# Kernel optimization log

Hardware: AMD Instinct MI355X
Metric: run time of the kernel (lower is better)

The kernel has to match this reference:

```python
import jax, jax.numpy as jnp
import numpy as np

B, S, D, E, R, TOP_K = 4, 4096, 1024, 10, 4, 2
SCALING = 1.0 / R  # alpha / rank


def setup_inputs() -> dict:
    key = jax.random.key(0)
    ks = jax.random.split(key, 7)
    return {
        "x": jax.random.normal(ks[0], (B, S, D), dtype=jnp.float32),
        "W_base": jax.random.normal(ks[1], (D, D), dtype=jnp.float32) * (D ** -0.5),
        "b_base": jax.random.normal(ks[2], (D,), dtype=jnp.float32) * 0.02,
        "gate_W": jax.random.normal(ks[3], (E, D), dtype=jnp.float32) * (D ** -0.5),
        "gate_b": jax.random.normal(ks[4], (E,), dtype=jnp.float32) * 0.02,
        "lora_down": jax.random.normal(ks[5], (E, R, D), dtype=jnp.float32) * (D ** -0.5),
        "lora_up": jax.random.normal(ks[6], (E, D, R), dtype=jnp.float32) * (R ** -0.5),
    }


def reference(x, W_base, b_base, gate_W, gate_b, lora_down, lora_up):
    # Base (frozen) linear: [B,S,D]
    base_out = jnp.einsum("bsd,od->bso", x, W_base) + b_base

    # Top-k gating: logits [B,S,E] -> sparse softmax weights [B,S,E]
    logits = jnp.einsum("bsd,ed->bse", x, gate_W) + gate_b
    top_vals, top_idx = jax.lax.top_k(logits, TOP_K)          # [B,S,K]
    top_w = jax.nn.softmax(top_vals, axis=-1)                 # [B,S,K]
    # scatter top-k weights back to dense [B,S,E] (non-top-k are zero)
    weights = jnp.sum(top_w[..., None] * jax.nn.one_hot(top_idx, E, dtype=x.dtype), axis=-2)

    # All-expert LoRA (matches original loop); weight in rank space to avoid
    # materializing [B,S,E,D]: sum_e w_e * up_e(down_e(x)) * scaling
    h = jnp.einsum("bsd,erd->bser", x, lora_down)             # [B,S,E,R]
    h = h * weights[..., None]
    lora_out = jnp.einsum("bser,edr->bsd", h, lora_up) * SCALING

    return base_out + lora_out
```

## Files before the change

kernel.cpp:

```cpp
#include <hip/hip_runtime.h>
#include <hip/hip_bf16.h>
#include <cstdint>
#include <cstddef>

#define D_DIM 1024
#define E_NUM 10

typedef __attribute__((ext_vector_type(8))) short bf16x8;
typedef __attribute__((ext_vector_type(4))) float f32x4;
typedef unsigned short u16;
typedef unsigned int u32;

__device__ __forceinline__ u16 f2bf(float f) {
  union { float f; u32 u; } v; v.f = f;
  u32 r = v.u + 0x7fffu + ((v.u >> 16) & 1u);
  return (u16)(r >> 16);
}
__device__ __forceinline__ float bf2f(u16 u) {
  union { u32 u; float f; } v; v.u = ((u32)u) << 16; return v.f;
}
__device__ __forceinline__ float dot4(float4 a, float4 b) {
  return a.x * b.x + a.y * b.y + a.z * b.z + a.w * b.w;
}

__global__ void conv_w(const float* __restrict__ W, u16* __restrict__ Wb) {
  const int i = (blockIdx.x * 256 + threadIdx.x) * 8;
  float4 a = *(const float4*)(W + i);
  float4 b = *(const float4*)(W + i + 4);
  *(ushort4*)(Wb + i)     = make_ushort4(f2bf(a.x), f2bf(a.y), f2bf(a.z), f2bf(a.w));
  *(ushort4*)(Wb + i + 4) = make_ushort4(f2bf(b.x), f2bf(b.y), f2bf(b.z), f2bf(b.w));
}

__global__ void prep_ldb(const float* __restrict__ ld, u16* __restrict__ Bld) {
  const int r = blockIdx.x;
  for (int c = threadIdx.x; c < D_DIM; c += 256)
    Bld[r * D_DIM + c] = (r < 40) ? f2bf(ld[r * D_DIM + c]) : (u16)0;
}

__global__ void prep_ub(const float* __restrict__ lup, u16* __restrict__ Ub) {
  const int g = blockIdx.x * 256 + threadIdx.x;
  const int o = g >> 6, j = g & 63;
  Ub[g] = (j < 40) ? f2bf(lup[(size_t)(j >> 2) * (D_DIM * 4) + o * 4 + (j & 3)]) : (u16)0;
}

__global__ __launch_bounds__(256)
void moe_prep_h(const float* __restrict__ x, const u16* __restrict__ Bld,
                u16* __restrict__ hb, u16* __restrict__ xb) {
  __shared__ u16 sX[4][16 * 64];
  __shared__ u16 sB[4][48 * 64];
  __shared__ float sP[4][3][16][17];

  const int tid = threadIdx.x, lane = tid & 63, w = tid >> 6;
  const int r0 = blockIdx.x * 16;
  const int kbase = w * 256;

  f32x4 acc[3] = {};

  float4 av[4];
#pragma unroll
  for (int i = 0; i < 2; ++i) {
    const int c = lane * 2 + i, row = c >> 3, kc = c & 7;
    const float* g = x + (size_t)(r0 + row) * D_DIM + kbase + kc * 8;
    av[i * 2]     = *(const float4*)g;
    av[i * 2 + 1] = *(const float4*)(g + 4);
  }

#pragma unroll 1
  for (int kt = 0; kt < 4; ++kt) {
    const int k0 = kbase + kt * 64;
#pragma unroll
    for (int i = 0; i < 6; ++i) {
      const int c = i * 64 + lane, row = c >> 3, kc = (c & 7) ^ (row & 7);
      __builtin_amdgcn_global_load_lds(
          (const __attribute__((address_space(1))) u32*)(Bld + (size_t)row * D_DIM + k0 + kc * 8),
          (__attribute__((address_space(3))) u32*)&sB[w][c * 8], 16, 0, 0);
    }
#pragma unroll
    for (int i = 0; i < 2; ++i) {
      const int c = lane * 2 + i, row = c >> 3, kc = c & 7;
      const float4 a = av[i * 2], b = av[i * 2 + 1];
      const ushort4 ha = make_ushort4(f2bf(a.x), f2bf(a.y), f2bf(a.z), f2bf(a.w));
      const ushort4 hb4 = make_ushort4(f2bf(b.x), f2bf(b.y), f2bf(b.z), f2bf(b.w));
      const int off = (row * 128 + kc * 16) ^ ((row & 7) << 4);
      *(ushort4*)((char*)sX[w] + off)     = ha;
      *(ushort4*)((char*)sX[w] + off + 8) = hb4;
      if (xb) {
        u16* dst = xb + (size_t)(r0 + row) * D_DIM + k0 + kc * 8;
        *(ushort4*)dst       = ha;
        *(ushort4*)(dst + 4) = hb4;
      }
    }
    __syncthreads();
    if (kt < 3) {
#pragma unroll
      for (int i = 0; i < 2; ++i) {
        const int c = lane * 2 + i, row = c >> 3, kc = c & 7;
        const float* g = x + (size_t)(r0 + row) * D_DIM + (k0 + 64) + kc * 8;
        av[i * 2]     = *(const float4*)g;
        av[i * 2 + 1] = *(const float4*)(g + 4);
      }
    }
#pragma unroll
    for (int kk = 0; kk < 2; ++kk) {
      const int kb = kk * 64 + ((lane >> 4) * 16);
      const int rA = lane & 15;
      const bf16x8 a0 = *(const bf16x8*)((const char*)sX[w] + ((rA * 128 + kb) ^ ((rA & 7) << 4)));
#pragma unroll
      for (int cf = 0; cf < 3; ++cf) {
        const int rB = cf * 16 + (lane & 15);
        const bf16x8 q = *(const bf16x8*)((const char*)sB[w] + ((rB * 128 + kb) ^ ((rB & 7) << 4)));
        acc[cf] = __builtin_amdgcn_mfma_f32_16x16x32_bf16(a0, q, acc[cf], 0, 0, 0);
      }
    }
    __syncthreads();
  }

#pragma unroll
  for (int cf = 0; cf < 3; ++cf)
#pragma unroll
    for (int j = 0; j < 4; ++j)
      sP[w][cf][(lane >> 4) * 4 + j][lane & 15] = acc[cf][j];
  __syncthreads();

  const int row = tid >> 4, c16 = tid & 15;
#pragma unroll
  for (int cf = 0; cf < 3; ++cf) {
    const int col = cf * 16 + c16;
    if (col < 40) {
      const float s = sP[0][cf][row][c16] + sP[1][cf][row][c16] +
                      sP[2][cf][row][c16] + sP[3][cf][row][c16];
      hb[(size_t)(r0 + row) * 40 + col] = f2bf(s);
    }
  }
}

__global__ __launch_bounds__(256, 2)
void moe_gate(const float* __restrict__ x, const float* __restrict__ gW,
              const float* __restrict__ gb, const u16* __restrict__ hb,
              u16* __restrict__ cd) {
  const int tid = threadIdx.x, lane = tid & 63, w = tid >> 6;
  const int tb = blockIdx.x * 16 + w * 4;

  float4 xv[4][4];
#pragma unroll
  for (int tok = 0; tok < 4; ++tok)
#pragma unroll
    for (int j = 0; j < 4; ++j)
      xv[tok][j] = *(const float4*)(x + (size_t)(tb + tok) * D_DIM + j * 256 + lane * 4);

  float lg[4][E_NUM];
#pragma unroll
  for (int e = 0; e < E_NUM; ++e) {
    float a0 = 0.f, a1 = 0.f, a2 = 0.f, a3 = 0.f;
#pragma unroll
    for (int j = 0; j < 4; ++j) {
      const float4 wv = *(const float4*)(gW + e * D_DIM + j * 256 + lane * 4);
      a0 += dot4(xv[0][j], wv);
      a1 += dot4(xv[1][j], wv);
      a2 += dot4(xv[2][j], wv);
      a3 += dot4(xv[3][j], wv);
    }
#pragma unroll
    for (int o = 32; o; o >>= 1) {
      a0 += __shfl_xor(a0, o);
      a1 += __shfl_xor(a1, o);
      a2 += __shfl_xor(a2, o);
      a3 += __shfl_xor(a3, o);
    }
    const float be = gb[e];
    lg[0][e] = a0 + be;
    lg[1][e] = a1 + be;
    lg[2][e] = a2 + be;
    lg[3][e] = a3 + be;
  }

  if (lane < 4) {
    const int tok = lane, t = tb + tok;
    int e0 = 0; float v0 = lg[tok][0];
#pragma unroll
    for (int e = 1; e < E_NUM; ++e) if (lg[tok][e] > v0) { v0 = lg[tok][e]; e0 = e; }
    int e1 = -1; float v1 = -3.0e38f;
#pragma unroll
    for (int e = 0; e < E_NUM; ++e) if (e != e0 && lg[tok][e] > v1) { v1 = lg[tok][e]; e1 = e; }
    const float pp = expf(v1 - v0);
    const float inv = 1.f / (1.f + pp);
    const float s0 = inv * 0.25f, s1 = pp * inv * 0.25f;

    u16* dst = cd + (size_t)t * 64;
    const u16* hrow = hb + (size_t)t * 40;
#pragma unroll
    for (int e = 0; e < E_NUM; ++e) {
      const float we = (e == e0) ? s0 : ((e == e1) ? s1 : 0.f);
      const ushort4 hh = *(const ushort4*)(hrow + e * 4);
      *(ushort4*)(dst + e * 4) = make_ushort4(
          f2bf(bf2f(hh.x) * we), f2bf(bf2f(hh.y) * we),
          f2bf(bf2f(hh.z) * we), f2bf(bf2f(hh.w) * we));
    }
#pragma unroll
    for (int j = 40; j < 64; j += 4)
      *(ushort4*)(dst + j) = make_ushort4(0, 0, 0, 0);
  }
}

__global__ __launch_bounds__(256, 2)
void moe_gemm_t(const u16* __restrict__ xb, const u16* __restrict__ Wbf,
                const u16* __restrict__ cd, const u16* __restrict__ Ub,
                const float* __restrict__ bias, float* __restrict__ out) {
  __shared__ u16 Al[2][128 * 64];
  __shared__ u16 Bl[2][128 * 64];

  const int tid = threadIdx.x, lane = tid & 63, wid = tid >> 6;
  const int wm = wid >> 1, wn = wid & 1;
  const int p = blockIdx.x;
  const int cx = p & 7, q = p >> 3;
  const int nb = q & 7, mb = cx * 16 + (q >> 3);
  const int m0 = mb * 128, n0 = nb * 128;

  int sc_row[4], sc_kc[4];
#pragma unroll
  for (int i = 0; i < 4; ++i) {
    const int c = i * 256 + tid;
    sc_row[i] = c >> 3;
    sc_kc[i]  = (c & 7) ^ (sc_row[i] & 7);
  }

  f32x4 acc[4][4] = {};

  auto STAGE = [&](int buf, int ktile) {
    const u16* As; const u16* Bs; size_t str; int ko;
    if (ktile < 16) {
      As = xb + (size_t)m0 * D_DIM; Bs = Wbf + (size_t)n0 * D_DIM;
      str = D_DIM; ko = ktile * 64;
    } else {
      As = cd + (size_t)m0 * 64; Bs = Ub + (size_t)n0 * 64;
      str = 64; ko = 0;
    }
#pragma unroll
    for (int i = 0; i < 4; ++i) {
      const int c = i * 256 + tid;
      __builtin_amdgcn_global_load_lds(
          (const __attribute__((address_space(1))) u32*)(As + (size_t)sc_row[i] * str + ko + sc_kc[i] * 8),
          (__attribute__((address_space(3))) u32*)&Al[buf][c * 8], 16, 0, 0);
    }
#pragma unroll
    for (int i = 0; i < 4; ++i) {
      const int c = i * 256 + tid;
      __builtin_amdgcn_global_load_lds(
          (const __attribute__((address_space(1))) u32*)(Bs + (size_t)sc_row[i] * str + ko + sc_kc[i] * 8),
          (__attribute__((address_space(3))) u32*)&Bl[buf][c * 8], 16, 0, 0);
    }
  };

  STAGE(0, 0);
  __syncthreads();

#pragma unroll 1
  for (int kt = 0; kt < 17; ++kt) {
    const int cur = kt & 1;
    if (kt < 16) STAGE(cur ^ 1, kt + 1);
#pragma unroll
    for (int kk = 0; kk < 2; ++kk) {
      bf16x8 af[4], bfr[4];
      const int kb = kk * 64 + ((lane >> 4) * 16);
#pragma unroll
      for (int m = 0; m < 4; ++m) {
        const int row = wm * 64 + m * 16 + (lane & 15);
        af[m] = *(const bf16x8*)((const char*)Al[cur] + ((row * 128 + kb) ^ ((row & 7) << 4)));
      }
#pragma unroll
      for (int n = 0; n < 4; ++n) {
        const int row = wn * 64 + n * 16 + (lane & 15);
        bfr[n] = *(const bf16x8*)((const char*)Bl[cur] + ((row * 128 + kb) ^ ((row & 7) << 4)));
      }
#pragma unroll
      for (int m = 0; m < 4; ++m)
#pragma unroll
        for (int n = 0; n < 4; ++n)
          acc[m][n] = __builtin_amdgcn_mfma_f32_16x16x32_bf16(af[m], bfr[n], acc[m][n], 0, 0, 0);
    }
    __syncthreads();
  }

  const int rg = lane >> 4, cl = lane & 15;
  const int baser = m0 + wm * 64, basec = n0 + wn * 64;
  float bs[4];
#pragma unroll
  for (int n = 0; n < 4; ++n) bs[n] = bias[basec + n * 16 + cl];
#pragma unroll
  for (int m = 0; m < 4; ++m)
#pragma unroll
    for (int j = 0; j < 4; ++j) {
      const int rr = baser + m * 16 + rg * 4 + j;
#pragma unroll
      for (int n = 0; n < 4; ++n)
        out[(size_t)rr * D_DIM + basec + n * 16 + cl] = acc[m][n][j] + bs[n];
    }
}

extern "C" void kernel_launch(void* const* d_in, const int* in_sizes, int n_in,
                              void* d_out, int out_size, void* d_ws, size_t ws_size,
                              hipStream_t stream) {
  const float* x   = (const float*)d_in[0];
  const float* Wb_ = (const float*)d_in[1];
  const float* bb  = (const float*)d_in[2];
  const float* gW  = (const float*)d_in[3];
  const float* gb  = (const float*)d_in[4];
  const float* ld  = (const float*)d_in[5];
  const float* lup = (const float*)d_in[6];

  char* w = (char*)d_ws;
  u16* Wbf = (u16*)w;
  u16* Ub  = (u16*)(w + 2048ull * 1024);
  u16* Bld = (u16*)(w + 2176ull * 1024);
  u16* cd  = (u16*)(w + 2272ull * 1024);
  u16* hb  = (u16*)(w + 4320ull * 1024);
  u16* xb  = (u16*)(w + 5600ull * 1024);

  hipLaunchKernelGGL(conv_w,     dim3(512),  dim3(256), 0, stream, Wb_, Wbf);
  hipLaunchKernelGGL(prep_ldb,   dim3(48),   dim3(256), 0, stream, ld, Bld);
  hipLaunchKernelGGL(prep_ub,    dim3(256),  dim3(256), 0, stream, lup, Ub);
  hipLaunchKernelGGL(moe_prep_h, dim3(1024), dim3(256), 0, stream, x, Bld, hb, xb);
  hipLaunchKernelGGL(moe_gate,   dim3(1024), dim3(256), 0, stream, x, gW, gb, hb, cd);
  hipLaunchKernelGGL(moe_gemm_t, dim3(1024), dim3(256), 0, stream,
                     xb, Wbf, cd, Ub, bb, (float*)d_out);
}
```

Before: 119.3 us.

## Restructure gate kernel to one token per lane with LDS transpose and K-split

The gating kernel now has each block handle 64 tokens. Each wave covers a quarter of the hidden dimension, and each lane accumulates all expert logits for one token, which removes the per-expert cross-lane shuffle reductions. x tiles are staged through a swizzled shared-memory buffer to transpose them, with register prefetch of the next chunk. Partial sums from the four waves are combined in LDS before top-k selection. The cost is 64KB of LDS per block, fewer blocks (256), and gate-weight loads that are uniform across lanes but repeated per wave.

```diff
diff --git a/kernel.cpp b/kernel.cpp
--- a/kernel.cpp
+++ b/kernel.cpp
@@ -134,54 +134,81 @@
   }
 }
 
-__global__ __launch_bounds__(256, 2)
-void moe_gate(const float* __restrict__ x, const float* __restrict__ gW,
-              const float* __restrict__ gb, const u16* __restrict__ hb,
-              u16* __restrict__ cd) {
+__global__ __launch_bounds__(256)
+void moe_gate2(const float* __restrict__ x, const float* __restrict__ gW,
+               const float* __restrict__ gb, const u16* __restrict__ hb,
+               u16* __restrict__ cd) {
+  __shared__ char sXraw[4][16384];
   const int tid = threadIdx.x, lane = tid & 63, w = tid >> 6;
-  const int tb = blockIdx.x * 16 + w * 4;
-
-  float4 xv[4][4];
-#pragma unroll
-  for (int tok = 0; tok < 4; ++tok)
-#pragma unroll
-    for (int j = 0; j < 4; ++j)
-      xv[tok][j] = *(const float4*)(x + (size_t)(tb + tok) * D_DIM + j * 256 + lane * 4);
-
-  float lg[4][E_NUM];
-#pragma unroll
-  for (int e = 0; e < E_NUM; ++e) {
-    float a0 = 0.f, a1 = 0.f, a2 = 0.f, a3 = 0.f;
-#pragma unroll
-    for (int j = 0; j < 4; ++j) {
-      const float4 wv = *(const float4*)(gW + e * D_DIM + j * 256 + lane * 4);
-      a0 += dot4(xv[0][j], wv);
-      a1 += dot4(xv[1][j], wv);
-      a2 += dot4(xv[2][j], wv);
-      a3 += dot4(xv[3][j], wv);
-    }
-#pragma unroll
-    for (int o = 32; o; o >>= 1) {
-      a0 += __shfl_xor(a0, o);
-      a1 += __shfl_xor(a1, o);
-      a2 += __shfl_xor(a2, o);
-      a3 += __shfl_xor(a3, o);
-    }
-    const float be = gb[e];
-    lg[0][e] = a0 + be;
-    lg[1][e] = a1 + be;
-    lg[2][e] = a2 + be;
-    lg[3][e] = a3 + be;
-  }
-
-  if (lane < 4) {
-    const int tok = lane, t = tb + tok;
-    int e0 = 0; float v0 = lg[tok][0];
-#pragma unroll
-    for (int e = 1; e < E_NUM; ++e) if (lg[tok][e] > v0) { v0 = lg[tok][e]; e0 = e; }
+  const int r0 = blockIdx.x * 64;
+  const int kq = w * 256;
+
+  float acc[E_NUM] = {};
+
+  float4 pv[16];
+#pragma unroll
+  for (int i = 0; i < 16; ++i) {
+    const int g = i * 64 + lane, tok = g >> 4, f4 = g & 15;
+    pv[i] = *(const float4*)(x + (size_t)(r0 + tok) * D_DIM + kq + f4 * 4);
+  }
+
+#pragma unroll 1
+  for (int c = 0; c < 4; ++c) {
+    const int k0 = kq + c * 64;
+#pragma unroll
+    for (int i = 0; i < 16; ++i) {
+      const int g = i * 64 + lane, tok = g >> 4, f4 = g & 15;
+      const int off = tok * 256 + ((f4 * 16) ^ ((tok & 7) << 4));
+      *(float4*)(sXraw[w] + off) = pv[i];
+    }
+    float4 xr[16];
+#pragma unroll
+    for (int k4 = 0; k4 < 16; ++k4) {
+      const int off = lane * 256 + ((k4 * 16) ^ ((lane & 7) << 4));
+      xr[k4] = *(const float4*)(sXraw[w] + off);
+    }
+    if (c < 3) {
+#pragma unroll
+      for (int i = 0; i < 16; ++i) {
+        const int g = i * 64 + lane, tok = g >> 4, f4 = g & 15;
+        pv[i] = *(const float4*)(x + (size_t)(r0 + tok) * D_DIM + (k0 + 64) + f4 * 4);
+      }
+    }
+#pragma unroll
+    for (int e = 0; e < E_NUM; ++e) {
+      float s = acc[e];
+#pragma unroll
+      for (int k4 = 0; k4 < 16; ++k4) {
+        const float4 wv = *(const float4*)(gW + e * D_DIM + k0 + k4 * 4);
+        s += dot4(xr[k4], wv);
+      }
+      acc[e] = s;
+    }
+  }
+
+  {
+    float* sp = (float*)sXraw[w];
+#pragma unroll
+    for (int e = 0; e < E_NUM; ++e) sp[lane * 13 + e] = acc[e];
+  }
+  __syncthreads();
+
+  if (tid < 64) {
+    const int t = r0 + tid;
+    float lg[E_NUM];
+#pragma unroll
+    for (int e = 0; e < E_NUM; ++e) {
+      lg[e] = ((const float*)sXraw[0])[tid * 13 + e]
+            + ((const float*)sXraw[1])[tid * 13 + e]
+            + ((const float*)sXraw[2])[tid * 13 + e]
+            + ((const float*)sXraw[3])[tid * 13 + e] + gb[e];
+    }
+    int e0 = 0; float v0 = lg[0];
+#pragma unroll
+    for (int e = 1; e < E_NUM; ++e) if (lg[e] > v0) { v0 = lg[e]; e0 = e; }
     int e1 = -1; float v1 = -3.0e38f;
 #pragma unroll
-    for (int e = 0; e < E_NUM; ++e) if (e != e0 && lg[tok][e] > v1) { v1 = lg[tok][e]; e1 = e; }
+    for (int e = 0; e < E_NUM; ++e) if (e != e0 && lg[e] > v1) { v1 = lg[e]; e1 = e; }
     const float pp = expf(v1 - v0);
     const float inv = 1.f / (1.f + pp);
     const float s0 = inv * 0.25f, s1 = pp * inv * 0.25f;
@@ -320,7 +347,7 @@
   hipLaunchKernelGGL(prep_ldb,   dim3(48),   dim3(256), 0, stream, ld, Bld);
   hipLaunchKernelGGL(prep_ub,    dim3(256),  dim3(256), 0, stream, lup, Ub);
   hipLaunchKernelGGL(moe_prep_h, dim3(1024), dim3(256), 0, stream, x, Bld, hb, xb);
-  hipLaunchKernelGGL(moe_gate,   dim3(1024), dim3(256), 0, stream, x, gW, gb, hb, cd);
+  hipLaunchKernelGGL(moe_gate2,  dim3(256),  dim3(256), 0, stream, x, gW, gb, hb, cd);
   hipLaunchKernelGGL(moe_gemm_t, dim3(1024), dim3(256), 0, stream,
                      xb, Wbf, cd, Ub, bb, (float*)d_out);
 }
```

Result: slower. 123.9 us (+3.9%).

## Fuse gating logits and top-k weighting into the LoRA-down prep kernel

Applied to the files above, without the earlier changes.

Merges the separate gate kernel into the LoRA-down projection kernel. The gate logits are now accumulated from the fp32 x registers already loaded for the bf16 conversion, reduced through shared memory, and combined with the rank-space h kept in shared memory (now fp32, no longer rounded to bf16). This removes a second full read of x (64 MB), the hb round trip and one launch. The cost is more register pressure, redundant gate-weight loads per lane, and a serial top-k step done by only 16 threads.

```diff
diff --git a/kernel.cpp b/kernel.cpp
--- a/kernel.cpp
+++ b/kernel.cpp
@@ -44,17 +44,21 @@
 }
 
 __global__ __launch_bounds__(256)
-void moe_prep_h(const float* __restrict__ x, const u16* __restrict__ Bld,
-                u16* __restrict__ hb, u16* __restrict__ xb) {
+void prep_hg(const float* __restrict__ x, const u16* __restrict__ Bld,
+             const float* __restrict__ gW, const float* __restrict__ gb,
+             u16* __restrict__ cd, u16* __restrict__ xb) {
   __shared__ u16 sX[4][16 * 64];
   __shared__ u16 sB[4][48 * 64];
   __shared__ float sP[4][3][16][17];
+  float* const sLG = (float*)sB;
+  float* const sH  = (float*)sX;
 
   const int tid = threadIdx.x, lane = tid & 63, w = tid >> 6;
   const int r0 = blockIdx.x * 16;
   const int kbase = w * 256;
 
   f32x4 acc[3] = {};
+  float alg[E_NUM] = {};
 
   float4 av[4];
 #pragma unroll
@@ -79,7 +83,7 @@
     for (int i = 0; i < 2; ++i) {
       const int c = lane * 2 + i, row = c >> 3, kc = c & 7;
       const float4 a = av[i * 2], b = av[i * 2 + 1];
-      const ushort4 ha = make_ushort4(f2bf(a.x), f2bf(a.y), f2bf(a.z), f2bf(a.w));
+      const ushort4 ha  = make_ushort4(f2bf(a.x), f2bf(a.y), f2bf(a.z), f2bf(a.w));
       const ushort4 hb4 = make_ushort4(f2bf(b.x), f2bf(b.y), f2bf(b.z), f2bf(b.w));
       const int off = (row * 128 + kc * 16) ^ ((row & 7) << 4);
       *(ushort4*)((char*)sX[w] + off)     = ha;
@@ -90,6 +94,17 @@
         *(ushort4*)(dst + 4) = hb4;
       }
     }
+#pragma unroll
+    for (int i = 0; i < 2; ++i) {
+      const int c = lane * 2 + i, kc = c & 7;
+      const float* gwk = gW + k0 + kc * 8;
+#pragma unroll
+      for (int e = 0; e < E_NUM; ++e) {
+        const float4 w1 = *(const float4*)(gwk + e * D_DIM);
+        const float4 w2 = *(const float4*)(gwk + e * D_DIM + 4);
+        alg[e] += dot4(av[i * 2], w1) + dot4(av[i * 2 + 1], w2);
+      }
+    }
     __syncthreads();
     if (kt < 3) {
 #pragma unroll
@@ -120,81 +135,50 @@
 #pragma unroll
     for (int j = 0; j < 4; ++j)
       sP[w][cf][(lane >> 4) * 4 + j][lane & 15] = acc[cf][j];
+  {
+    float* dst = sLG + (size_t)(lane >> 2) * 160 + (w * 4 + (lane & 3)) * 10;
+#pragma unroll
+    for (int e = 0; e < E_NUM; ++e) dst[e] = alg[e];
+  }
   __syncthreads();
 
   const int row = tid >> 4, c16 = tid & 15;
 #pragma unroll
   for (int cf = 0; cf < 3; ++cf) {
     const int col = cf * 16 + c16;
-    if (col < 40) {
-      const float s = sP[0][cf][row][c16] + sP[1][cf][row][c16] +
-                      sP[2][cf][row][c16] + sP[3][cf][row][c16];
-      hb[(size_t)(r0 + row) * 40 + col] = f2bf(s);
-    }
-  }
-}
-
-__global__ __launch_bounds__(256, 2)
-void moe_gate(const float* __restrict__ x, const float* __restrict__ gW,
-              const float* __restrict__ gb, const u16* __restrict__ hb,
-              u16* __restrict__ cd) {
-  const int tid = threadIdx.x, lane = tid & 63, w = tid >> 6;
-  const int tb = blockIdx.x * 16 + w * 4;
-
-  float4 xv[4][4];
-#pragma unroll
-  for (int tok = 0; tok < 4; ++tok)
-#pragma unroll
-    for (int j = 0; j < 4; ++j)
-      xv[tok][j] = *(const float4*)(x + (size_t)(tb + tok) * D_DIM + j * 256 + lane * 4);
-
-  float lg[4][E_NUM];
-#pragma unroll
-  for (int e = 0; e < E_NUM; ++e) {
-    float a0 = 0.f, a1 = 0.f, a2 = 0.f, a3 = 0.f;
-#pragma unroll
-    for (int j = 0; j < 4; ++j) {
-      const float4 wv = *(const float4*)(gW + e * D_DIM + j * 256 + lane * 4);
-      a0 += dot4(xv[0][j], wv);
-      a1 += dot4(xv[1][j], wv);
-      a2 += dot4(xv[2][j], wv);
-      a3 += dot4(xv[3][j], wv);
-    }
-#pragma unroll
-    for (int o = 32; o; o >>= 1) {
-      a0 += __shfl_xor(a0, o);
-      a1 += __shfl_xor(a1, o);
-      a2 += __shfl_xor(a2, o);
-      a3 += __shfl_xor(a3, o);
-    }
-    const float be = gb[e];
-    lg[0][e] = a0 + be;
-    lg[1][e] = a1 + be;
-    lg[2][e] = a2 + be;
-    lg[3][e] = a3 + be;
-  }
-
-  if (lane < 4) {
-    const int tok = lane, t = tb + tok;
-    int e0 = 0; float v0 = lg[tok][0];
-#pragma unroll
-    for (int e = 1; e < E_NUM; ++e) if (lg[tok][e] > v0) { v0 = lg[tok][e]; e0 = e; }
+    if (col < 40)
+      sH[row * 41 + col] = sP[0][cf][row][c16] + sP[1][cf][row][c16] +
+                           sP[2][cf][row][c16] + sP[3][cf][row][c16];
+  }
+  __syncthreads();
+
+  if (tid < 16) {
+    const int t = r0 + tid;
+    float lg[E_NUM];
+#pragma unroll
+    for (int e = 0; e < E_NUM; ++e) {
+      float s = gb[e];
+#pragma unroll
+      for (int p = 0; p < 16; ++p) s += sLG[tid * 160 + p * 10 + e];
+      lg[e] = s;
+    }
+    int e0 = 0; float v0 = lg[0];
+#pragma unroll
+    for (int e = 1; e < E_NUM; ++e) if (lg[e] > v0) { v0 = lg[e]; e0 = e; }
     int e1 = -1; float v1 = -3.0e38f;
 #pragma unroll
-    for (int e = 0; e < E_NUM; ++e) if (e != e0 && lg[tok][e] > v1) { v1 = lg[tok][e]; e1 = e; }
+    for (int e = 0; e < E_NUM; ++e) if (e != e0 && lg[e] > v1) { v1 = lg[e]; e1 = e; }
     const float pp = expf(v1 - v0);
     const float inv = 1.f / (1.f + pp);
     const float s0 = inv * 0.25f, s1 = pp * inv * 0.25f;
 
     u16* dst = cd + (size_t)t * 64;
-    const u16* hrow = hb + (size_t)t * 40;
 #pragma unroll
     for (int e = 0; e < E_NUM; ++e) {
       const float we = (e == e0) ? s0 : ((e == e1) ? s1 : 0.f);
-      const ushort4 hh = *(const ushort4*)(hrow + e * 4);
+      const float* hr = sH + tid * 41 + e * 4;
       *(ushort4*)(dst + e * 4) = make_ushort4(
-          f2bf(bf2f(hh.x) * we), f2bf(bf2f(hh.y) * we),
-          f2bf(bf2f(hh.z) * we), f2bf(bf2f(hh.w) * we));
+          f2bf(hr[0] * we), f2bf(hr[1] * we), f2bf(hr[2] * we), f2bf(hr[3] * we));
     }
 #pragma unroll
     for (int j = 40; j < 64; j += 4)
@@ -313,14 +297,12 @@
   u16* Ub  = (u16*)(w + 2048ull * 1024);
   u16* Bld = (u16*)(w + 2176ull * 1024);
   u16* cd  = (u16*)(w + 2272ull * 1024);
-  u16* hb  = (u16*)(w + 4320ull * 1024);
   u16* xb  = (u16*)(w + 5600ull * 1024);
 
-  hipLaunchKernelGGL(conv_w,     dim3(512),  dim3(256), 0, stream, Wb_, Wbf);
-  hipLaunchKernelGGL(prep_ldb,   dim3(48),   dim3(256), 0, stream, ld, Bld);
-  hipLaunchKernelGGL(prep_ub,    dim3(256),  dim3(256), 0, stream, lup, Ub);
-  hipLaunchKernelGGL(moe_prep_h, dim3(1024), dim3(256), 0, stream, x, Bld, hb, xb);
-  hipLaunchKernelGGL(moe_gate,   dim3(1024), dim3(256), 0, stream, x, gW, gb, hb, cd);
+  hipLaunchKernelGGL(conv_w,   dim3(512),  dim3(256), 0, stream, Wb_, Wbf);
+  hipLaunchKernelGGL(prep_ldb, dim3(48),   dim3(256), 0, stream, ld, Bld);
+  hipLaunchKernelGGL(prep_ub,  dim3(256),  dim3(256), 0, stream, lup, Ub);
+  hipLaunchKernelGGL(prep_hg,  dim3(1024), dim3(256), 0, stream, x, Bld, gW, gb, cd, xb);
   hipLaunchKernelGGL(moe_gemm_t, dim3(1024), dim3(256), 0, stream,
                      xb, Wbf, cd, Ub, bb, (float*)d_out);
 }
```

After: 128.4 us. 7.7% more time.
